# Kernel tuning notes

Measured on AMD Instinct MI355X. Metric: run time of the kernel, lower is better.

The kernel has to match this reference:

```python
import jax, jax.numpy as jnp
import numpy as np

N_NODES = 100000
N_EDGES = 1600000
IN_CH = 64
HID = 64
OUT_CH = 3
N_LAYERS = 4


def gcn_conv(x, src, dst, norm, W, b):
    # x: [N, d_in]; W: [d_in, d_out]; norm: [E'] (per-edge symmetric norm)
    h = x @ W                               # [N, d_out]
    msgs = h[src] * norm[:, None]           # [E', d_out] gather + scale
    out = jax.ops.segment_sum(msgs, dst, num_segments=N_NODES)  # scatter-add
    return out + b


def build_graph(edge_index):
    # PyG GCNConv default: add self-loops, symmetric normalization
    loops = jnp.arange(N_NODES, dtype=edge_index.dtype)
    src = jnp.concatenate([edge_index[0], loops])
    dst = jnp.concatenate([edge_index[1], loops])
    deg = jax.ops.segment_sum(jnp.ones_like(dst, dtype=jnp.float32), dst,
                              num_segments=N_NODES)
    dinv = jnp.where(deg > 0, jax.lax.rsqrt(jnp.maximum(deg, 1e-12)), 0.0)
    norm = dinv[src] * dinv[dst]            # [E + N]
    return src, dst, norm


def setup_inputs() -> dict:
    key = jax.random.key(0)
    ks = jax.random.split(key, 5)
    x = jax.random.normal(ks[0], (N_NODES, IN_CH), dtype=jnp.float32)
    edge_index = jax.random.randint(ks[1], (2, N_EDGES), 0, N_NODES, dtype=jnp.int64)
    Ws = jax.random.normal(ks[2], (N_LAYERS, HID, HID), dtype=jnp.float32) * (1.0 / np.sqrt(HID))
    bs = jnp.zeros((N_LAYERS, HID), dtype=jnp.float32)
    Wc = jax.random.normal(ks[3], (HID, OUT_CH), dtype=jnp.float32) * (1.0 / np.sqrt(HID))
    bc = jnp.zeros((OUT_CH,), dtype=jnp.float32)
    return {"x": x, "edge_index": edge_index, "Ws": Ws, "bs": bs, "Wc": Wc, "bc": bc}


def reference(x, edge_index, Ws, bs, Wc, bc):
    src, dst, norm = build_graph(edge_index)
    for i in range(N_LAYERS):
        x_new = gcn_conv(x, src, dst, norm, Ws[i], bs[i])
        # residual when i > 0 and feature dims match (always true: hidden->hidden)
        x = x + x_new if i > 0 else x_new
        x = jax.nn.relu(x)
        # dropout is identity in eval mode (training=False)
    return x @ Wc + bc
```

## Files before the change

### kernel.cpp

```cpp
#include <hip/hip_runtime.h>
#include <hip/hip_fp16.h>

#define NN 100000
#define HD 64
#define NB ((NN + 255) >> 8)
#define P1_CHUNK 8192

__global__ __launch_bounds__(256) void hist_kernel(const int* __restrict__ dst,
                                                   int* __restrict__ bcnt, int E) {
    __shared__ int hist[NB];
    int t = threadIdx.x;
    int e0 = blockIdx.x * P1_CHUNK;
    int count = min(P1_CHUNK, E - e0);
    for (int b = t; b < NB; b += 256) hist[b] = 0;
    __syncthreads();
    for (int i = t; i < count; i += 256) atomicAdd(&hist[dst[e0 + i] >> 8], 1);
    __syncthreads();
    for (int b = t; b < NB; b += 256) {
        int c = hist[b];
        if (c) atomicAdd(&bcnt[b], c);
    }
}

__global__ void bscan_kernel(const int* __restrict__ bcnt, int* __restrict__ boff,
                             int* __restrict__ bcur, int* __restrict__ row_ptr,
                             int E, int n) {
    __shared__ int sm[512];
    int t = threadIdx.x;
    int v = (t < NB) ? bcnt[t] : 0;
    sm[t] = v;
    __syncthreads();
    for (int off = 1; off < 512; off <<= 1) {
        int u = (t >= off) ? sm[t - off] : 0;
        __syncthreads();
        sm[t] += u;
        __syncthreads();
    }
    if (t < NB) {
        boff[t] = sm[t] - v;
        bcur[t] = sm[t] - v;
    }
    if (t == 0) {
        boff[NB] = E;
        row_ptr[n] = E;
    }
}

__global__ __launch_bounds__(256) void p1_kernel(const int* __restrict__ src,
                                                 const int* __restrict__ dst,
                                                 int* __restrict__ bcur,
                                                 int2* __restrict__ ebuf, int E) {
    __shared__ int hist[NB];
    __shared__ int cur[NB];
    int t = threadIdx.x;
    int e0 = blockIdx.x * P1_CHUNK;
    int count = min(P1_CHUNK, E - e0);
    for (int b = t; b < NB; b += 256) hist[b] = 0;
    __syncthreads();
    for (int i = t; i < count; i += 256) atomicAdd(&hist[dst[e0 + i] >> 8], 1);
    __syncthreads();
    for (int b = t; b < NB; b += 256) {
        int c = hist[b];
        cur[b] = c ? atomicAdd(&bcur[b], c) : 0;
    }
    __syncthreads();
    for (int i = t; i < count; i += 256) {
        int d = dst[e0 + i], s = src[e0 + i];
        int pos = atomicAdd(&cur[d >> 8], 1);
        ebuf[pos] = make_int2(d, s);
    }
}

__global__ __launch_bounds__(256) void p2_kernel(const int2* __restrict__ ebuf,
                                                 const int* __restrict__ boff,
                                                 int* __restrict__ row_ptr,
                                                 float* __restrict__ dinv,
                                                 int* __restrict__ csr_src, int n) {
    __shared__ int cnt[256];
    __shared__ int cur[256];
    int b = blockIdx.x;
    int node0 = b << 8;
    int t = threadIdx.x;
    int beg = boff[b], end = boff[b + 1];
    cnt[t] = 0;
    __syncthreads();
    for (int i = beg + t; i < end; i += 256) atomicAdd(&cnt[ebuf[i].x - node0], 1);
    __syncthreads();
    int deg = cnt[t];
    for (int off = 1; off < 256; off <<= 1) {
        int v = (t >= off) ? cnt[t - off] : 0;
        __syncthreads();
        cnt[t] += v;
        __syncthreads();
    }
    int excl = cnt[t] - deg;
    int node = node0 + t;
    if (node < n) {
        row_ptr[node] = beg + excl;
        dinv[node] = rsqrtf((float)deg + 1.0f);
    }
    cur[t] = beg + excl;
    __syncthreads();
    for (int i = beg + t; i < end; i += 256) {
        int2 p = ebuf[i];
        int pos = atomicAdd(&cur[p.x - node0], 1);
        csr_src[pos] = p.y;
    }
}

__global__ __launch_bounds__(256) void matmul64_kernel(const float* __restrict__ X,
                                                       const float* __restrict__ W,
                                                       const float* __restrict__ dinv,
                                                       float2* __restrict__ H, int n) {
    __shared__ float Wl[64 * 64];
    __shared__ float Xs[64 * 65];
    int tid = threadIdx.x;
    int row0 = blockIdx.x * 64;
    const float4* W4 = (const float4*)W;
    float4* Wl4 = (float4*)Wl;
#pragma unroll
    for (int i = 0; i < 4; ++i) Wl4[tid + 256 * i] = W4[tid + 256 * i];
#pragma unroll
    for (int i = 0; i < 4; ++i) {
        int l = tid + 256 * i;
        int r = l >> 4, k0 = (l & 15) * 4;
        int row = row0 + r;
        float4 xv = (row < n) ? ((const float4*)X)[(size_t)row * 16 + (l & 15)]
                              : make_float4(0.f, 0.f, 0.f, 0.f);
        Xs[r * 65 + k0 + 0] = xv.x;
        Xs[r * 65 + k0 + 1] = xv.y;
        Xs[r * 65 + k0 + 2] = xv.z;
        Xs[r * 65 + k0 + 3] = xv.w;
    }
    __syncthreads();
    int tx = tid & 15, ty = tid >> 4;
    float acc[4][4] = {};
    const float4* Wlr4 = (const float4*)Wl;
#pragma unroll 4
    for (int k = 0; k < 64; ++k) {
        float4 b = Wlr4[k * 16 + tx];
        float a0 = Xs[(ty * 4 + 0) * 65 + k];
        float a1 = Xs[(ty * 4 + 1) * 65 + k];
        float a2 = Xs[(ty * 4 + 2) * 65 + k];
        float a3 = Xs[(ty * 4 + 3) * 65 + k];
        acc[0][0] += a0 * b.x; acc[0][1] += a0 * b.y; acc[0][2] += a0 * b.z; acc[0][3] += a0 * b.w;
        acc[1][0] += a1 * b.x; acc[1][1] += a1 * b.y; acc[1][2] += a1 * b.z; acc[1][3] += a1 * b.w;
        acc[2][0] += a2 * b.x; acc[2][1] += a2 * b.y; acc[2][2] += a2 * b.z; acc[2][3] += a2 * b.w;
        acc[3][0] += a3 * b.x; acc[3][1] += a3 * b.y; acc[3][2] += a3 * b.z; acc[3][3] += a3 * b.w;
    }
#pragma unroll
    for (int j = 0; j < 4; ++j) {
        int row = row0 + ty * 4 + j;
        if (row < n) {
            float dn = dinv[row];
            __half2 p01 = __float22half2_rn(make_float2(acc[j][0] * dn, acc[j][1] * dn));
            __half2 p23 = __float22half2_rn(make_float2(acc[j][2] * dn, acc[j][3] * dn));
            float2 st;
            st.x = *reinterpret_cast<float*>(&p01);
            st.y = *reinterpret_cast<float*>(&p23);
            H[(size_t)row * 16 + tx] = st;
        }
    }
}

#define UNPACK_ACC(A, RAW) do {                                              \
    __half2 _h01 = *reinterpret_cast<__half2*>(&(RAW).x);                    \
    __half2 _h23 = *reinterpret_cast<__half2*>(&(RAW).y);                    \
    float2 _f01 = __half22float2(_h01);                                      \
    float2 _f23 = __half22float2(_h23);                                      \
    (A).x += _f01.x; (A).y += _f01.y; (A).z += _f23.x; (A).w += _f23.y;      \
} while (0)

__global__ void agg_kernel(const float2* __restrict__ h2, const int* __restrict__ row_ptr,
                           const int* __restrict__ csr_src, const float* __restrict__ dinv,
                           const float* __restrict__ b, const float* __restrict__ xprev,
                           float* __restrict__ xout, float* __restrict__ outp,
                           const float* __restrict__ Wc, const float* __restrict__ bc,
                           int n, int residual, int project) {
    int lane = threadIdx.x & 63;
    int q = lane >> 4, c4 = lane & 15;
    int wid = (blockIdx.x * blockDim.x + threadIdx.x) >> 6;
    int node = wid * 4 + q;
    bool active = node < n;
    int nc = active ? node : 0;
    int beg = row_ptr[nc], end = row_ptr[nc + 1];
    int cnt = end - beg;
    float4 acc = make_float4(0.f, 0.f, 0.f, 0.f);
    {
        float2 raw = h2[(size_t)nc * 16 + c4];
        UNPACK_ACC(acc, raw);
    }
    int base = q * 16;
    for (int k = 0; k < cnt; k += 16) {
        int p = beg + k + c4;
        int sv = (p < end) ? csr_src[p] : 0;
        int m = min(16, cnt - k);
        int i = 0;
        for (; i + 8 <= m; i += 8) {
            int s0 = __shfl(sv, base + i + 0);
            int s1 = __shfl(sv, base + i + 1);
            int s2 = __shfl(sv, base + i + 2);
            int s3 = __shfl(sv, base + i + 3);
            int s4 = __shfl(sv, base + i + 4);
            int s5 = __shfl(sv, base + i + 5);
            int s6 = __shfl(sv, base + i + 6);
            int s7 = __shfl(sv, base + i + 7);
            float2 v0 = h2[(size_t)s0 * 16 + c4];
            float2 v1 = h2[(size_t)s1 * 16 + c4];
            float2 v2 = h2[(size_t)s2 * 16 + c4];
            float2 v3 = h2[(size_t)s3 * 16 + c4];
            float2 v4 = h2[(size_t)s4 * 16 + c4];
            float2 v5 = h2[(size_t)s5 * 16 + c4];
            float2 v6 = h2[(size_t)s6 * 16 + c4];
            float2 v7 = h2[(size_t)s7 * 16 + c4];
            UNPACK_ACC(acc, v0); UNPACK_ACC(acc, v1); UNPACK_ACC(acc, v2); UNPACK_ACC(acc, v3);
            UNPACK_ACC(acc, v4); UNPACK_ACC(acc, v5); UNPACK_ACC(acc, v6); UNPACK_ACC(acc, v7);
        }
        for (; i + 4 <= m; i += 4) {
            int s0 = __shfl(sv, base + i + 0);
            int s1 = __shfl(sv, base + i + 1);
            int s2 = __shfl(sv, base + i + 2);
            int s3 = __shfl(sv, base + i + 3);
            float2 v0 = h2[(size_t)s0 * 16 + c4];
            float2 v1 = h2[(size_t)s1 * 16 + c4];
            float2 v2 = h2[(size_t)s2 * 16 + c4];
            float2 v3 = h2[(size_t)s3 * 16 + c4];
            UNPACK_ACC(acc, v0); UNPACK_ACC(acc, v1); UNPACK_ACC(acc, v2); UNPACK_ACC(acc, v3);
        }
        for (; i < m; ++i) {
            int s = __shfl(sv, base + i);
            float2 hv = h2[(size_t)s * 16 + c4];
            UNPACK_ACC(acc, hv);
        }
    }
    if (active) {
        float dn = dinv[node];
        float4 bb = ((const float4*)b)[c4];
        float4 v;
        v.x = acc.x * dn + bb.x; v.y = acc.y * dn + bb.y;
        v.z = acc.z * dn + bb.z; v.w = acc.w * dn + bb.w;
        if (residual) {
            float4 r = ((const float4*)xprev)[(size_t)node * 16 + c4];
            v.x += r.x; v.y += r.y; v.z += r.z; v.w += r.w;
        }
        v.x = fmaxf(v.x, 0.f); v.y = fmaxf(v.y, 0.f);
        v.z = fmaxf(v.z, 0.f); v.w = fmaxf(v.w, 0.f);
        if (!project) {
            ((float4*)xout)[(size_t)node * 16 + c4] = v;
        } else {
            int cb = c4 * 4;
#pragma unroll
            for (int j = 0; j < 3; ++j) {
                float p = v.x * Wc[(cb + 0) * 3 + j] + v.y * Wc[(cb + 1) * 3 + j] +
                          v.z * Wc[(cb + 2) * 3 + j] + v.w * Wc[(cb + 3) * 3 + j];
                p += __shfl_down(p, 8);
                p += __shfl_down(p, 4);
                p += __shfl_down(p, 2);
                p += __shfl_down(p, 1);
                if (c4 == 0) outp[node * 3 + j] = p + bc[j];
            }
        }
    }
}

extern "C" void kernel_launch(void* const* d_in, const int* in_sizes, int n_in,
                              void* d_out, int out_size, void* d_ws, size_t ws_size,
                              hipStream_t stream) {
    const float* x  = (const float*)d_in[0];
    const int*   ei = (const int*)d_in[1];
    const float* Ws = (const float*)d_in[2];
    const float* bs = (const float*)d_in[3];
    const float* Wc = (const float*)d_in[4];
    const float* bc = (const float*)d_in[5];
    float* out = (float*)d_out;

    int E = in_sizes[1] / 2;
    const int* src = ei;
    const int* dst = ei + E;
    int nchunks = (E + P1_CHUNK - 1) / P1_CHUNK;

    char* wsb = (char*)d_ws;
    size_t off = 0;
    int*   bcnt    = (int*)(wsb + off); off += 512 * 4;
    int*   boff    = (int*)(wsb + off); off += 512 * 4;
    int*   bcur    = (int*)(wsb + off); off += 512 * 4;
    int*   row_ptr = (int*)(wsb + off); off += 100608 * 4;
    float* dinv    = (float*)(wsb + off); off += 100352 * 4;
    int*   csr_src = (int*)(wsb + off); off += ((size_t)E + 256) * 4;
    int2*  ebuf    = (int2*)(wsb + off); off += (size_t)E * 8;
    float2* h      = (float2*)(wsb + off); off += (size_t)NN * HD * 2;
    float* xa      = (float*)(wsb + off); off += (size_t)NN * HD * 4;
    float* xb      = (float*)(wsb + off); off += (size_t)NN * HD * 4;

    hipMemsetAsync(bcnt, 0, 512 * sizeof(int), stream);
    hist_kernel<<<nchunks, 256, 0, stream>>>(dst, bcnt, E);
    bscan_kernel<<<1, 512, 0, stream>>>(bcnt, boff, bcur, row_ptr, E, NN);
    p1_kernel<<<nchunks, 256, 0, stream>>>(src, dst, bcur, ebuf, E);
    p2_kernel<<<NB, 256, 0, stream>>>(ebuf, boff, row_ptr, dinv, csr_src, NN);

    const float* xin = x;
    float* bufs[2] = {xa, xb};
    int agg_blocks = ((NN + 3) / 4 * 64 + 255) / 256;
    for (int l = 0; l < 4; ++l) {
        float* xout = bufs[l & 1];
        matmul64_kernel<<<(NN + 63) / 64, 256, 0, stream>>>(
            xin, Ws + (size_t)l * HD * HD, dinv, h, NN);
        agg_kernel<<<agg_blocks, 256, 0, stream>>>(
            h, row_ptr, csr_src, dinv, bs + l * HD, xin, xout,
            out, Wc, bc, NN, l > 0, l == 3);
        xin = xout;
    }
}
```

Before: 346.8 us.

## Aggregate in packed half2 with 8 lanes per node and 16-byte gathers

The aggregation kernel now gives each node 8 lanes instead of 16. Each lane gathers a 16-byte float4 holding 8 half values and accumulates with packed __hadd2 instead of converting each neighbour to fp32. The intent is fewer, wider loads and half the ALU work per gathered element, with 8 nodes handled per wave. Accumulating in fp16 risks precision loss and overflow for high-degree nodes. Fewer lanes per node also lowers per-node parallelism.

```diff
diff --git a/kernel.cpp b/kernel.cpp
--- a/kernel.cpp
+++ b/kernel.cpp
@@ -163,101 +163,119 @@
     }
 }
 
-#define UNPACK_ACC(A, RAW) do {                                              \
-    __half2 _h01 = *reinterpret_cast<__half2*>(&(RAW).x);                    \
-    __half2 _h23 = *reinterpret_cast<__half2*>(&(RAW).y);                    \
-    float2 _f01 = __half22float2(_h01);                                      \
-    float2 _f23 = __half22float2(_h23);                                      \
-    (A).x += _f01.x; (A).y += _f01.y; (A).z += _f23.x; (A).w += _f23.y;      \
+#define PK_ACC(RAW) do {                                                     \
+    a0 = __hadd2(a0, *reinterpret_cast<__half2*>(&(RAW).x));                 \
+    a1 = __hadd2(a1, *reinterpret_cast<__half2*>(&(RAW).y));                 \
+    a2 = __hadd2(a2, *reinterpret_cast<__half2*>(&(RAW).z));                 \
+    a3 = __hadd2(a3, *reinterpret_cast<__half2*>(&(RAW).w));                 \
 } while (0)
 
-__global__ void agg_kernel(const float2* __restrict__ h2, const int* __restrict__ row_ptr,
+__global__ void agg_kernel(const float4* __restrict__ h4, const int* __restrict__ row_ptr,
                            const int* __restrict__ csr_src, const float* __restrict__ dinv,
                            const float* __restrict__ b, const float* __restrict__ xprev,
                            float* __restrict__ xout, float* __restrict__ outp,
                            const float* __restrict__ Wc, const float* __restrict__ bc,
                            int n, int residual, int project) {
     int lane = threadIdx.x & 63;
-    int q = lane >> 4, c4 = lane & 15;
+    int o = lane >> 3, c8 = lane & 7;
     int wid = (blockIdx.x * blockDim.x + threadIdx.x) >> 6;
-    int node = wid * 4 + q;
+    int node = wid * 8 + o;
     bool active = node < n;
     int nc = active ? node : 0;
     int beg = row_ptr[nc], end = row_ptr[nc + 1];
     int cnt = end - beg;
-    float4 acc = make_float4(0.f, 0.f, 0.f, 0.f);
+    __half2 a0, a1, a2, a3;
     {
-        float2 raw = h2[(size_t)nc * 16 + c4];
-        UNPACK_ACC(acc, raw);
-    }
-    int base = q * 16;
-    for (int k = 0; k < cnt; k += 16) {
-        int p = beg + k + c4;
+        float4 sv = h4[(size_t)nc * 8 + c8];
+        a0 = *reinterpret_cast<__half2*>(&sv.x);
+        a1 = *reinterpret_cast<__half2*>(&sv.y);
+        a2 = *reinterpret_cast<__half2*>(&sv.z);
+        a3 = *reinterpret_cast<__half2*>(&sv.w);
+    }
+    int base = o * 8;
+    for (int k = 0; k < cnt; k += 8) {
+        int p = beg + k + c8;
         int sv = (p < end) ? csr_src[p] : 0;
-        int m = min(16, cnt - k);
-        int i = 0;
-        for (; i + 8 <= m; i += 8) {
-            int s0 = __shfl(sv, base + i + 0);
-            int s1 = __shfl(sv, base + i + 1);
-            int s2 = __shfl(sv, base + i + 2);
-            int s3 = __shfl(sv, base + i + 3);
-            int s4 = __shfl(sv, base + i + 4);
-            int s5 = __shfl(sv, base + i + 5);
-            int s6 = __shfl(sv, base + i + 6);
-            int s7 = __shfl(sv, base + i + 7);
-            float2 v0 = h2[(size_t)s0 * 16 + c4];
-            float2 v1 = h2[(size_t)s1 * 16 + c4];
-            float2 v2 = h2[(size_t)s2 * 16 + c4];
-            float2 v3 = h2[(size_t)s3 * 16 + c4];
-            float2 v4 = h2[(size_t)s4 * 16 + c4];
-            float2 v5 = h2[(size_t)s5 * 16 + c4];
-            float2 v6 = h2[(size_t)s6 * 16 + c4];
-            float2 v7 = h2[(size_t)s7 * 16 + c4];
-            UNPACK_ACC(acc, v0); UNPACK_ACC(acc, v1); UNPACK_ACC(acc, v2); UNPACK_ACC(acc, v3);
-            UNPACK_ACC(acc, v4); UNPACK_ACC(acc, v5); UNPACK_ACC(acc, v6); UNPACK_ACC(acc, v7);
-        }
-        for (; i + 4 <= m; i += 4) {
-            int s0 = __shfl(sv, base + i + 0);
-            int s1 = __shfl(sv, base + i + 1);
-            int s2 = __shfl(sv, base + i + 2);
-            int s3 = __shfl(sv, base + i + 3);
-            float2 v0 = h2[(size_t)s0 * 16 + c4];
-            float2 v1 = h2[(size_t)s1 * 16 + c4];
-            float2 v2 = h2[(size_t)s2 * 16 + c4];
-            float2 v3 = h2[(size_t)s3 * 16 + c4];
-            UNPACK_ACC(acc, v0); UNPACK_ACC(acc, v1); UNPACK_ACC(acc, v2); UNPACK_ACC(acc, v3);
-        }
-        for (; i < m; ++i) {
-            int s = __shfl(sv, base + i);
-            float2 hv = h2[(size_t)s * 16 + c4];
-            UNPACK_ACC(acc, hv);
+        int m = min(8, cnt - k);
+        if (m == 8) {
+            int s0 = __shfl(sv, base + 0);
+            int s1 = __shfl(sv, base + 1);
+            int s2 = __shfl(sv, base + 2);
+            int s3 = __shfl(sv, base + 3);
+            int s4 = __shfl(sv, base + 4);
+            int s5 = __shfl(sv, base + 5);
+            int s6 = __shfl(sv, base + 6);
+            int s7 = __shfl(sv, base + 7);
+            float4 v0 = h4[(size_t)s0 * 8 + c8];
+            float4 v1 = h4[(size_t)s1 * 8 + c8];
+            float4 v2 = h4[(size_t)s2 * 8 + c8];
+            float4 v3 = h4[(size_t)s3 * 8 + c8];
+            float4 v4 = h4[(size_t)s4 * 8 + c8];
+            float4 v5 = h4[(size_t)s5 * 8 + c8];
+            float4 v6 = h4[(size_t)s6 * 8 + c8];
+            float4 v7 = h4[(size_t)s7 * 8 + c8];
+            PK_ACC(v0); PK_ACC(v1); PK_ACC(v2); PK_ACC(v3);
+            PK_ACC(v4); PK_ACC(v5); PK_ACC(v6); PK_ACC(v7);
+        } else {
+            int i = 0;
+            for (; i + 4 <= m; i += 4) {
+                int s0 = __shfl(sv, base + i + 0);
+                int s1 = __shfl(sv, base + i + 1);
+                int s2 = __shfl(sv, base + i + 2);
+                int s3 = __shfl(sv, base + i + 3);
+                float4 v0 = h4[(size_t)s0 * 8 + c8];
+                float4 v1 = h4[(size_t)s1 * 8 + c8];
+                float4 v2 = h4[(size_t)s2 * 8 + c8];
+                float4 v3 = h4[(size_t)s3 * 8 + c8];
+                PK_ACC(v0); PK_ACC(v1); PK_ACC(v2); PK_ACC(v3);
+            }
+            for (; i < m; ++i) {
+                int s = __shfl(sv, base + i);
+                float4 hv = h4[(size_t)s * 8 + c8];
+                PK_ACC(hv);
+            }
         }
     }
     if (active) {
         float dn = dinv[node];
-        float4 bb = ((const float4*)b)[c4];
-        float4 v;
-        v.x = acc.x * dn + bb.x; v.y = acc.y * dn + bb.y;
-        v.z = acc.z * dn + bb.z; v.w = acc.w * dn + bb.w;
+        float2 f0 = __half22float2(a0);
+        float2 f1 = __half22float2(a1);
+        float2 f2 = __half22float2(a2);
+        float2 f3 = __half22float2(a3);
+        const float4* b4 = (const float4*)b;
+        float4 bb0 = b4[c8 * 2], bb1 = b4[c8 * 2 + 1];
+        float4 u, w;
+        u.x = f0.x * dn + bb0.x; u.y = f0.y * dn + bb0.y;
+        u.z = f1.x * dn + bb0.z; u.w = f1.y * dn + bb0.w;
+        w.x = f2.x * dn + bb1.x; w.y = f2.y * dn + bb1.y;
+        w.z = f3.x * dn + bb1.z; w.w = f3.y * dn + bb1.w;
         if (residual) {
-            float4 r = ((const float4*)xprev)[(size_t)node * 16 + c4];
-            v.x += r.x; v.y += r.y; v.z += r.z; v.w += r.w;
+            const float4* xp4 = (const float4*)xprev;
+            float4 r0 = xp4[(size_t)node * 16 + c8 * 2];
+            float4 r1 = xp4[(size_t)node * 16 + c8 * 2 + 1];
+            u.x += r0.x; u.y += r0.y; u.z += r0.z; u.w += r0.w;
+            w.x += r1.x; w.y += r1.y; w.z += r1.z; w.w += r1.w;
         }
-        v.x = fmaxf(v.x, 0.f); v.y = fmaxf(v.y, 0.f);
-        v.z = fmaxf(v.z, 0.f); v.w = fmaxf(v.w, 0.f);
+        u.x = fmaxf(u.x, 0.f); u.y = fmaxf(u.y, 0.f);
+        u.z = fmaxf(u.z, 0.f); u.w = fmaxf(u.w, 0.f);
+        w.x = fmaxf(w.x, 0.f); w.y = fmaxf(w.y, 0.f);
+        w.z = fmaxf(w.z, 0.f); w.w = fmaxf(w.w, 0.f);
         if (!project) {
-            ((float4*)xout)[(size_t)node * 16 + c4] = v;
+            float4* xo4 = (float4*)xout;
+            xo4[(size_t)node * 16 + c8 * 2] = u;
+            xo4[(size_t)node * 16 + c8 * 2 + 1] = w;
         } else {
-            int cb = c4 * 4;
+            int cb = c8 * 8;
 #pragma unroll
             for (int j = 0; j < 3; ++j) {
-                float p = v.x * Wc[(cb + 0) * 3 + j] + v.y * Wc[(cb + 1) * 3 + j] +
-                          v.z * Wc[(cb + 2) * 3 + j] + v.w * Wc[(cb + 3) * 3 + j];
-                p += __shfl_down(p, 8);
-                p += __shfl_down(p, 4);
-                p += __shfl_down(p, 2);
-                p += __shfl_down(p, 1);
-                if (c4 == 0) outp[node * 3 + j] = p + bc[j];
+                float p = u.x * Wc[(cb + 0) * 3 + j] + u.y * Wc[(cb + 1) * 3 + j] +
+                          u.z * Wc[(cb + 2) * 3 + j] + u.w * Wc[(cb + 3) * 3 + j] +
+                          w.x * Wc[(cb + 4) * 3 + j] + w.y * Wc[(cb + 5) * 3 + j] +
+                          w.z * Wc[(cb + 6) * 3 + j] + w.w * Wc[(cb + 7) * 3 + j];
+                p += __shfl_down(p, 4, 8);
+                p += __shfl_down(p, 2, 8);
+                p += __shfl_down(p, 1, 8);
+                if (c8 == 0) outp[node * 3 + j] = p + bc[j];
             }
         }
     }
@@ -300,13 +318,13 @@
 
     const float* xin = x;
     float* bufs[2] = {xa, xb};
-    int agg_blocks = ((NN + 3) / 4 * 64 + 255) / 256;
+    int agg_blocks = ((NN + 7) / 8 * 64 + 255) / 256;
     for (int l = 0; l < 4; ++l) {
         float* xout = bufs[l & 1];
         matmul64_kernel<<<(NN + 63) / 64, 256, 0, stream>>>(
             xin, Ws + (size_t)l * HD * HD, dinv, h, NN);
         agg_kernel<<<agg_blocks, 256, 0, stream>>>(
-            h, row_ptr, csr_src, dinv, bs + l * HD, xin, xout,
+            (const float4*)h, row_ptr, csr_src, dinv, bs + l * HD, xin, xout,
             out, Wc, bc, NN, l > 0, l == 3);
         xin = xout;
     }
```

Result: no change. 347.2 us (+0.1%).
